# Kernel tuning notes

Hardware: AMD Instinct MI355X
Metric: run time of the kernel (lower is better)

Reference implementation:

```python
import jax, jax.numpy as jnp
import numpy as np

B, S, D, H, HD = 2, 2048, 1024, 16, 64
LN_EPS = 1e-6


def setup_inputs() -> dict:
    key = jax.random.key(0)
    ks = jax.random.split(key, 4)
    x = jax.random.normal(ks[0], (B, S, D), dtype=jnp.float32)
    ln_scale = jnp.ones((D,), jnp.float32)
    ln_bias = jnp.zeros((D,), jnp.float32)
    w_qkv = jax.random.normal(ks[1], (D, H, 3 * HD), jnp.float32) * (D ** -0.5)
    b_qkv = jnp.zeros((H, 3 * HD), jnp.float32)
    w_out = jax.random.normal(ks[2], (H, HD, D), jnp.float32) * ((H * HD) ** -0.5)
    b_out = jnp.zeros((D,), jnp.float32)
    # causal mask, broadcastable to weights shape [B, H, q, k]
    mask = jnp.tril(jnp.ones((S, S), dtype=bool))[None, None, :, :]
    return {"x": x, "ln_scale": ln_scale, "ln_bias": ln_bias,
            "w_qkv": w_qkv, "b_qkv": b_qkv, "w_out": w_out, "b_out": b_out,
            "mask": mask}


def _attention_block(x, ln_scale, ln_bias, w_qkv, b_qkv, w_out, b_out, mask):
    # Pre-LayerNorm
    mu = jnp.mean(x, axis=-1, keepdims=True)
    var = jnp.mean(jnp.square(x - mu), axis=-1, keepdims=True)
    xn = (x - mu) * jax.lax.rsqrt(var + LN_EPS) * ln_scale + ln_bias
    # QKV projection: [B,S,D] x [D,H,3*hd] -> [B,S,H,3*hd]
    qkv = jnp.einsum('bsd,dhf->bshf', xn, w_qkv) + b_qkv
    q, k, v = jnp.split(qkv, 3, axis=-1)  # each [B,S,H,hd]
    # scaled dot-product attention in float32 (softmax_dtype)
    scale = HD ** -0.5
    qf = (q * scale).astype(jnp.float32)
    kf = k.astype(jnp.float32)
    weights = jnp.einsum('bqhd,bkhd->bhqk', qf, kf)  # [B,H,S,S]
    weights = jnp.where(mask, weights, jnp.finfo(jnp.float32).min)
    weights = jax.nn.softmax(weights, axis=-1).astype(x.dtype)
    attn = jnp.einsum('bhqk,bkhd->bqhd', weights, v)  # [B,S,H,hd]
    # output projection, contracting (H, hd)
    out = jnp.einsum('bqhd,hdf->bqf', attn, w_out) + b_out  # [B,S,D]
    return out


def reference(x, ln_scale, ln_bias, w_qkv, b_qkv, w_out, b_out, mask):
    return _attention_block(x, ln_scale, ln_bias, w_qkv, b_qkv, w_out, b_out, mask)
```

## Files before the change

### kernel.cpp

```cpp
#include <hip/hip_runtime.h>
#include <hip/hip_bf16.h>
#include <stdint.h>

#define B_ 2
#define S_ 2048
#define D_ 1024
#define H_ 16
#define HD_ 64
#define M_ (B_*S_)
#define NQKV_ (H_*3*HD_)

typedef __attribute__((ext_vector_type(8))) short short8;
typedef __attribute__((ext_vector_type(4))) float f32x4;
typedef unsigned short u16;
typedef unsigned int u32;

__device__ __forceinline__ u16 f2b(float f){
  u32 u = __float_as_uint(f);
  u32 r = (u + 0x7FFFu + ((u >> 16) & 1u)) >> 16;
  return (u16)r;
}

__device__ __forceinline__ float exp2v(float x){
  float r; asm("v_exp_f32 %0, %1" : "=v"(r) : "v"(x)); return r;
}

__device__ __forceinline__ void gl_lds16(const void* g, void* l){
  __builtin_amdgcn_global_load_lds(
      (const __attribute__((address_space(1))) void*)g,
      (__attribute__((address_space(3))) void*)l, 16, 0, 0);
}

__global__ __launch_bounds__(256) void ln_kernel(const float* __restrict__ x,
    const float* __restrict__ gam, const float* __restrict__ bet, u16* __restrict__ xn){
  int row = blockIdx.x;
  const float4* xr = (const float4*)(x + (size_t)row * D_);
  float4 v = xr[threadIdx.x];
  float s = v.x + v.y + v.z + v.w;
  float q = v.x*v.x + v.y*v.y + v.z*v.z + v.w*v.w;
  #pragma unroll
  for(int o = 32; o > 0; o >>= 1){ s += __shfl_down(s, o); q += __shfl_down(q, o); }
  __shared__ float red[8];
  int w = threadIdx.x >> 6, lane = threadIdx.x & 63;
  if(lane == 0){ red[w] = s; red[4+w] = q; }
  __syncthreads();
  float st = red[0]+red[1]+red[2]+red[3];
  float qt = red[4]+red[5]+red[6]+red[7];
  float mu = st * (1.0f / D_);
  float inv = rsqrtf(qt * (1.0f / D_) - mu*mu + 1e-6f);
  float4 g = ((const float4*)gam)[threadIdx.x];
  float4 b = ((const float4*)bet)[threadIdx.x];
  ushort4 o4;
  o4.x = f2b((v.x-mu)*inv*g.x + b.x);
  o4.y = f2b((v.y-mu)*inv*g.y + b.y);
  o4.z = f2b((v.z-mu)*inv*g.z + b.z);
  o4.w = f2b((v.w-mu)*inv*g.w + b.w);
  ((ushort4*)(xn + (size_t)row * D_))[threadIdx.x] = o4;
}

__global__ __launch_bounds__(256) void tconv_kernel(const float* __restrict__ src,
    u16* __restrict__ dst, int R, int C){
  __shared__ float tile[64][65];
  int tx = threadIdx.x & 63, ty = threadIdx.x >> 6;
  int r0 = blockIdx.y * 64, c0 = blockIdx.x * 64;
  #pragma unroll
  for(int i = 0; i < 16; i++){
    int r = ty*16 + i;
    tile[r][tx] = src[(size_t)(r0+r)*C + c0 + tx];
  }
  __syncthreads();
  #pragma unroll
  for(int i = 0; i < 16; i++){
    int r = ty*16 + i;
    dst[(size_t)(c0+r)*R + r0 + tx] = f2b(tile[tx][r]);
  }
}

__global__ __launch_bounds__(256) void vtrans_kernel(const u16* __restrict__ V, u16* __restrict__ Vt){
  __shared__ u16 t2[64][66];
  int tx = threadIdx.x & 63, ty = threadIdx.x >> 6;
  int bh = blockIdx.y, s0 = blockIdx.x * 64;
  const u16* src = V + (size_t)bh * S_ * HD_;
  u16* dst = Vt + (size_t)bh * HD_ * S_;
  #pragma unroll
  for(int i = 0; i < 16; i++){
    int r = ty*16 + i;
    t2[r][tx] = src[(size_t)(s0+r)*HD_ + tx];
  }
  __syncthreads();
  #pragma unroll
  for(int i = 0; i < 16; i++){
    int hd = ty*16 + i;
    dst[(size_t)hd*S_ + s0 + tx] = t2[tx][hd];
  }
}

__global__ __launch_bounds__(512, 2) void gemm256_kernel(const u16* __restrict__ A,
    const u16* __restrict__ Bt, const float* __restrict__ bias,
    u16* __restrict__ o0, u16* __restrict__ o1, u16* __restrict__ o2){
  constexpr int K_ = 1024;
  __shared__ __align__(16) char smem[131072];
  int tid = threadIdx.x, w = tid >> 6, lane = tid & 63;
  int wm = w >> 2, wn = w & 3;
  int bid = blockIdx.y * gridDim.x + blockIdx.x;
  int nwg = gridDim.x * gridDim.y;
  int cpx = nwg >> 3;
  int swz = (bid & 7) * cpx + (bid >> 3);
  int m0 = (swz / gridDim.x) * 256, n0 = (swz % gridDim.x) * 256;

  f32x4 z = {0.f, 0.f, 0.f, 0.f};
  f32x4 acc[8][4];
  #pragma unroll
  for(int r = 0; r < 8; r++)
    #pragma unroll
    for(int c = 0; c < 4; c++) acc[r][c] = z;

  int srow_lo = w*8 + (lane >> 3);
  int sch = (lane & 7) ^ (srow_lo & 7);
  auto STAGE_A = [&](int buf, int half, int kt){
    #pragma unroll
    for(int l = 0; l < 2; l++){
      int row = l*64 + srow_lo;
      gl_lds16(A + (size_t)(m0 + half*128 + row)*K_ + kt*64 + sch*8,
               smem + (buf*2 + half)*16384 + l*8192 + w*1024);
    }
  };
  auto STAGE_B = [&](int buf, int half, int kt){
    #pragma unroll
    for(int l = 0; l < 2; l++){
      int row = l*64 + srow_lo;
      gl_lds16(Bt + (size_t)(n0 + half*128 + row)*K_ + kt*64 + sch*8,
               smem + 65536 + (buf*2 + half)*16384 + l*8192 + w*1024);
    }
  };

  int ln15 = lane & 15, g = lane >> 4;
  int co0 = ((g    ) ^ (ln15 & 7)) * 16;
  int co1 = ((4 + g) ^ (ln15 & 7)) * 16;
  auto LDA = [&](int buf, int r, int k)->short8{
    int byt = buf*32768 + wm*16384 + (r*16 + ln15)*128 + (k ? co1 : co0);
    return *(const short8*)(smem + byt);
  };
  auto LDB = [&](int buf, int c, int k)->short8{
    int byt = 65536 + buf*32768 + (wn >> 1)*16384
            + ((wn & 1)*64 + c*16 + ln15)*128 + (k ? co1 : co0);
    return *(const short8*)(smem + byt);
  };
  #define BAR()   __builtin_amdgcn_s_barrier()
  #define LGKM0() do{ asm volatile("s_waitcnt lgkmcnt(0)" ::: "memory"); \
                      __builtin_amdgcn_sched_barrier(0); }while(0)

  constexpr int nk = K_ / 64;
  STAGE_A(0, 0, 0); STAGE_A(0, 1, 0);
  STAGE_B(0, 0, 0); STAGE_B(0, 1, 0);
  STAGE_B(1, 0, 1); STAGE_B(1, 1, 1);
  asm volatile("s_waitcnt vmcnt(4)" ::: "memory");
  __builtin_amdgcn_sched_barrier(0);
  BAR();

  #pragma unroll 2
  for(int t = 0; t < nk; t++){
    int buf = t & 1;
    int kA = (t + 1 < nk) ? t + 1 : nk - 1;
    int kB = (t + 2 < nk) ? t + 2 : nk - 1;
    short8 a0[4][2], a1[4][2], b0[2][2], b1[2][2];
    #pragma unroll
    for(int r = 0; r < 4; r++){ a0[r][0] = LDA(buf, r, 0); a0[r][1] = LDA(buf, r, 1); }
    #pragma unroll
    for(int c = 0; c < 2; c++){ b0[c][0] = LDB(buf, c, 0); b0[c][1] = LDB(buf, c, 1); }
    STAGE_A(buf ^ 1, 0, kA);
    BAR(); LGKM0();
    __builtin_amdgcn_s_setprio(1);
    #pragma unroll
    for(int r = 0; r < 4; r++)
      #pragma unroll
      for(int c = 0; c < 2; c++){
        acc[r][c] = __builtin_amdgcn_mfma_f32_16x16x32_bf16(a0[r][0], b0[c][0], acc[r][c], 0, 0, 0);
        acc[r][c] = __builtin_amdgcn_mfma_f32_16x16x32_bf16(a0[r][1], b0[c][1], acc[r][c], 0, 0, 0);
      }
    __builtin_amdgcn_s_setprio(0);
    BAR();
    #pragma unroll
    for(int c = 0; c < 2; c++){ b1[c][0] = LDB(buf, c + 2, 0); b1[c][1] = LDB(buf, c + 2, 1); }
    STAGE_A(buf ^ 1, 1, kA);
    BAR(); LGKM0();
    __builtin_amdgcn_s_setprio(1);
    #pragma unroll
    for(int r = 0; r < 4; r++)
      #pragma unroll
      for(int c = 0; c < 2; c++){
        acc[r][c+2] = __builtin_amdgcn_mfma_f32_16x16x32_bf16(a0[r][0], b1[c][0], acc[r][c+2], 0, 0, 0);
        acc[r][c+2] = __builtin_amdgcn_mfma_f32_16x16x32_bf16(a0[r][1], b1[c][1], acc[r][c+2], 0, 0, 0);
      }
    __builtin_amdgcn_s_setprio(0);
    BAR();
    #pragma unroll
    for(int r = 0; r < 4; r++){ a1[r][0] = LDA(buf, r + 4, 0); a1[r][1] = LDA(buf, r + 4, 1); }
    STAGE_B(buf, 0, kB);
    BAR(); LGKM0();
    __builtin_amdgcn_s_setprio(1);
    #pragma unroll
    for(int r = 0; r < 4; r++)
      #pragma unroll
      for(int c = 0; c < 2; c++){
        acc[r+4][c+2] = __builtin_amdgcn_mfma_f32_16x16x32_bf16(a1[r][0], b1[c][0], acc[r+4][c+2], 0, 0, 0);
        acc[r+4][c+2] = __builtin_amdgcn_mfma_f32_16x16x32_bf16(a1[r][1], b1[c][1], acc[r+4][c+2], 0, 0, 0);
      }
    __builtin_amdgcn_s_setprio(0);
    BAR();
    STAGE_B(buf, 1, kB);
    BAR();
    __builtin_amdgcn_s_setprio(1);
    #pragma unroll
    for(int r = 0; r < 4; r++)
      #pragma unroll
      for(int c = 0; c < 2; c++){
        acc[r+4][c] = __builtin_amdgcn_mfma_f32_16x16x32_bf16(a1[r][0], b0[c][0], acc[r+4][c], 0, 0, 0);
        acc[r+4][c] = __builtin_amdgcn_mfma_f32_16x16x32_bf16(a1[r][1], b0[c][1], acc[r+4][c], 0, 0, 0);
      }
    __builtin_amdgcn_s_setprio(0);
    asm volatile("s_waitcnt vmcnt(4)" ::: "memory");
    __builtin_amdgcn_sched_barrier(0);
    BAR();
  }
  #undef BAR
  #undef LGKM0

  #pragma unroll
  for(int r = 0; r < 8; r++){
    #pragma unroll
    for(int c = 0; c < 4; c++){
      #pragma unroll
      for(int q = 0; q < 4; q++){
        int row = m0 + wm*128 + r*16 + g*4 + q;
        int col = n0 + wn*64 + c*16 + ln15;
        float v = acc[r][c][q] + bias[col];
        int h = col / 192, rr = col - h*192;
        int b = row >> 11, s = row & (S_ - 1);
        size_t base = ((size_t)(b*H_ + h)*S_ + s) * HD_;
        if(rr < 64)        o0[base + rr]       = f2b(v * 0.180336884f);
        else if(rr < 128)  o1[base + rr - 64]  = f2b(v);
        else               o2[base + rr - 128] = f2b(v);
      }
    }
  }
}

__global__ __launch_bounds__(256) void gemm_kernel(const u16* __restrict__ A,
    const u16* __restrict__ Bt, const float* __restrict__ bias,
    float* __restrict__ out, int K, int N){
  __shared__ u16 As[2][128*32];
  __shared__ u16 Bs[2][128*32];
  int tid = threadIdx.x, w = tid >> 6, lane = tid & 63;
  int bid = blockIdx.y * gridDim.x + blockIdx.x;
  int nwg = gridDim.x * gridDim.y;
  int cpx = nwg >> 3;
  int swz = (bid & 7) * cpx + (bid >> 3);
  int m0 = (swz / gridDim.x) * 128, n0 = (swz % gridDim.x) * 128;
  int wm = w >> 1, wn = w & 1;
  f32x4 z = {0.f, 0.f, 0.f, 0.f};
  f32x4 acc[4][4];
  #pragma unroll
  for(int r = 0; r < 4; r++)
    #pragma unroll
    for(int c = 0; c < 4; c++) acc[r][c] = z;
  int srow = lane >> 2, sch = (lane & 3) * 8;
  const u16* Ag = A + (size_t)m0 * K + (size_t)srow * K + sch;
  const u16* Bg = Bt + (size_t)n0 * K + (size_t)srow * K + sch;

  auto STAGE = [&](int buf, int kt){
    #pragma unroll
    for(int i = 0; i < 2; i++){
      int rb = w*32 + i*16;
      gl_lds16(Ag + (size_t)rb*K + kt, &As[buf][rb*32]);
      gl_lds16(Bg + (size_t)rb*K + kt, &Bs[buf][rb*32]);
    }
  };

  int nk = K >> 5;
  STAGE(0, 0);
  asm volatile("s_waitcnt vmcnt(0)" ::: "memory");
  __builtin_amdgcn_sched_barrier(0);
  __builtin_amdgcn_s_barrier();
  for(int t = 0; t < nk; t++){
    int cur = t & 1;
    if(t + 1 < nk){
      STAGE(cur ^ 1, (t + 1) * 32);
      asm volatile("s_waitcnt vmcnt(4)" ::: "memory");
    } else {
      asm volatile("s_waitcnt vmcnt(0)" ::: "memory");
    }
    __builtin_amdgcn_sched_barrier(0);
    __builtin_amdgcn_s_barrier();
    int kc = (lane >> 4) * 8;
    int ar = wm*64 + (lane & 15);
    int bc = wn*64 + (lane & 15);
    short8 af[4], bfr[4];
    #pragma unroll
    for(int r = 0; r < 4; r++) af[r] = *(const short8*)&As[cur][(ar + r*16)*32 + kc];
    #pragma unroll
    for(int c = 0; c < 4; c++) bfr[c] = *(const short8*)&Bs[cur][(bc + c*16)*32 + kc];
    __builtin_amdgcn_s_setprio(1);
    #pragma unroll
    for(int r = 0; r < 4; r++)
      #pragma unroll
      for(int c = 0; c < 4; c++)
        acc[r][c] = __builtin_amdgcn_mfma_f32_16x16x32_bf16(af[r], bfr[c], acc[r][c], 0, 0, 0);
    __builtin_amdgcn_s_setprio(0);
    asm volatile("" ::: "memory");
    __builtin_amdgcn_s_barrier();
  }

  #pragma unroll
  for(int r = 0; r < 4; r++){
    #pragma unroll
    for(int c = 0; c < 4; c++){
      #pragma unroll
      for(int q = 0; q < 4; q++){
        int row = m0 + wm*64 + r*16 + (lane >> 4)*4 + q;
        int col = n0 + wn*64 + c*16 + (lane & 15);
        out[(size_t)row * N + col] = acc[r][c][q] + bias[col];
      }
    }
  }
}


template<int HALF>
__device__ __forceinline__ void compute_tile(
    const char* KsB, const char* VsB, char* Pw, const short8* qf,
    f32x4* o, float& m_run, float& l_run, bool diag, int lane, int wr){
  constexpr int KB0 = (HALF == 1) ? 2 : 0;
  constexpr int KBN = (HALF == -1) ? 4 : 2;
  f32x4 z = {0.f, 0.f, 0.f, 0.f};
  f32x4 sf[4];
  __builtin_amdgcn_s_setprio(1);
  #pragma unroll
  for(int kb = KB0; kb < KB0 + KBN; kb++){
    f32x4 acc = z;
    #pragma unroll
    for(int c = 0; c < 2; c++){
      int row = kb*16 + (lane & 15);
      int kc16 = (lane >> 4) + c*4;
      short8 kf = *(const short8*)(KsB + row*128 + ((kc16 ^ (row & 7)) * 16));
      acc = __builtin_amdgcn_mfma_f32_16x16x32_bf16(kf, qf[c], acc, 0, 0, 0);
    }
    sf[kb] = acc;
  }
  __builtin_amdgcn_s_setprio(0);
  if(diag){
    int qo = wr*16 + (lane & 15);
    #pragma unroll
    for(int kb = KB0; kb < KB0 + KBN; kb++)
      #pragma unroll
      for(int r = 0; r < 4; r++){
        int kvo = kb*16 + (lane >> 4)*4 + r;
        if(kvo > qo) sf[kb][r] = -1e30f;
      }
  }
  int g = lane >> 4;
  float pmax = -1e28f;
  #pragma unroll
  for(int kb = KB0; kb < KB0 + KBN; kb++)
    pmax = fmaxf(pmax, fmaxf(fmaxf(sf[kb][0], sf[kb][1]), fmaxf(sf[kb][2], sf[kb][3])));
  pmax = fmaxf(pmax, __shfl_xor(pmax, 16));
  pmax = fmaxf(pmax, __shfl_xor(pmax, 32));
  if(!__all(pmax <= m_run + 8.f)){
    float mn = fmaxf(m_run, pmax);
    float al = exp2v(m_run - mn);
    m_run = mn;
    l_run *= al;
    float alr[4];
    #pragma unroll
    for(int r = 0; r < 4; r++) alr[r] = __shfl(al, g*4 + r);
    #pragma unroll
    for(int n = 0; n < 4; n++)
      #pragma unroll
      for(int r = 0; r < 4; r++) o[n][r] *= alr[r];
  }
  float p[4][4];
  float sum = 0.f;
  #pragma unroll
  for(int kb = KB0; kb < KB0 + KBN; kb++){
    #pragma unroll
    for(int r = 0; r < 4; r++) p[kb][r] = exp2v(sf[kb][r] - m_run);
    sum += (p[kb][0]+p[kb][1]) + (p[kb][2]+p[kb][3]);
  }
  sum += __shfl_xor(sum, 16);
  sum += __shfl_xor(sum, 32);
  l_run += sum;
  int qrow = lane & 15;
  #pragma unroll
  for(int kb = KB0; kb < KB0 + KBN; kb++){
    u32 lo, hi;
    asm("v_cvt_pk_bf16_f32 %0, %1, %2" : "=v"(lo) : "v"(p[kb][0]), "v"(p[kb][1]));
    asm("v_cvt_pk_bf16_f32 %0, %1, %2" : "=v"(hi) : "v"(p[kb][2]), "v"(p[kb][3]));
    uint2 pk; pk.x = lo; pk.y = hi;
    int byt = (qrow*128 + kb*32 + g*8) ^ ((qrow & 7) << 4);
    *(uint2*)(Pw + byt) = pk;
  }
  constexpr int C0 = (HALF == 1) ? 1 : 0;
  constexpr int C1 = (HALF == 0) ? 0 : 1;
  __builtin_amdgcn_s_setprio(1);
  #pragma unroll
  for(int c = C0; c <= C1; c++){
    int prow = lane & 15;
    int kb16 = ((lane >> 4) + c*4) * 16;
    short8 pa = *(const short8*)(Pw + ((prow*128 + kb16) ^ ((prow & 7) << 4)));
    #pragma unroll
    for(int n = 0; n < 4; n++){
      int vrow = n*16 + (lane & 15);
      int kc16 = (lane >> 4) + c*4;
      short8 vf = *(const short8*)(VsB + vrow*128 + ((kc16 ^ (vrow & 7)) * 16));
      o[n] = __builtin_amdgcn_mfma_f32_16x16x32_bf16(pa, vf, o[n], 0, 0, 0);
    }
  }
  __builtin_amdgcn_s_setprio(0);
}

__global__ __launch_bounds__(512) void attn_kernel(const u16* __restrict__ Q,
    const u16* __restrict__ Kb, const u16* __restrict__ Vt, u16* __restrict__ O){
  __shared__ __align__(16) char smem[49152];
  char* PsBase = smem + 32768;
  int tid = threadIdx.x, w = tid >> 6, lane = tid & 63;
  int wr = w & 3, role = w >> 2;
  int L = blockIdx.x;
  int pi = (L >> 3) & 15;
  int bh = (L & 7) + 8 * (L >> 7);
  const int NT = S_ / 64;
  int ta = pi, tb = NT - 1 - pi;
  const u16* Qg = Q + (size_t)bh * S_ * HD_;
  const u16* Kg = Kb + (size_t)bh * S_ * HD_;
  const u16* Vg = Vt + (size_t)bh * HD_ * S_;
  int b = bh >> 4, h = bh & 15;

  short8 qb[2], qa[2];
  {
    int rb_ = tb*64 + wr*16 + (lane & 15);
    #pragma unroll
    for(int c = 0; c < 2; c++)
      qb[c] = *(const short8*)(Qg + (size_t)rb_*HD_ + (lane >> 4)*8 + c*32);
    if(role == 1){
      int ra_ = ta*64 + wr*16 + (lane & 15);
      #pragma unroll
      for(int c = 0; c < 2; c++)
        qa[c] = *(const short8*)(Qg + (size_t)ra_*HD_ + (lane >> 4)*8 + c*32);
    }
  }
  f32x4 z = {0.f, 0.f, 0.f, 0.f};
  f32x4 o[4];
  float m_run = -1e30f, l_run = 0.f;
  #pragma unroll
  for(int i = 0; i < 4; i++) o[i] = z;
  int svrow = lane >> 3, scb = lane & 7;

  auto STAGE = [&](int buf, int kt){
    int kv0 = kt * 64;
    int rowblk = w * 8;
    int row = rowblk + svrow;
    int cbs = scb ^ (row & 7);
    gl_lds16(Kg + (size_t)(kv0 + row)*HD_ + cbs*8, smem + buf*8192 + rowblk*128);
    gl_lds16(Vg + (size_t)row*S_ + kv0 + cbs*8, smem + 16384 + buf*8192 + rowblk*128);
  };

  STAGE(0, 0);
  asm volatile("s_waitcnt vmcnt(0)" ::: "memory");
  __builtin_amdgcn_sched_barrier(0);
  __builtin_amdgcn_s_barrier();
  int cur = 0;
  char* Pw = PsBase + w*2048;
  for(int kt = 0; kt <= tb; kt++){
    if(kt < tb){
      STAGE(cur ^ 1, kt + 1);
      asm volatile("s_waitcnt vmcnt(2)" ::: "memory");
    } else {
      asm volatile("s_waitcnt vmcnt(0)" ::: "memory");
    }
    __builtin_amdgcn_sched_barrier(0);
    __builtin_amdgcn_s_barrier();
    const char* KsB = (const char*)(smem + cur*8192);
    const char* VsB = (const char*)(smem + 16384 + cur*8192);
    if(role == 0){
      if(kt <= ta) compute_tile<-1>(KsB, VsB, Pw, qb, o, m_run, l_run, false, lane, wr);
      else         compute_tile<0>(KsB, VsB, Pw, qb, o, m_run, l_run, kt == tb, lane, wr);
    } else {
      if(kt <= ta){
        compute_tile<-1>(KsB, VsB, Pw, qa, o, m_run, l_run, kt == ta, lane, wr);
        if(kt == ta){
          float linv = 1.f / l_run;
          float invr[4];
          #pragma unroll
          for(int r = 0; r < 4; r++) invr[r] = __shfl(linv, (lane >> 4)*4 + r);
          #pragma unroll
          for(int n = 0; n < 4; n++)
            #pragma unroll
            for(int r = 0; r < 4; r++){
              int s = ta*64 + wr*16 + (lane >> 4)*4 + r;
              int hd = n*16 + (lane & 15);
              O[(((size_t)(b*S_ + s))*H_ + h)*HD_ + hd] = f2b(o[n][r] * invr[r]);
            }
          m_run = -1e30f; l_run = 0.f;
          #pragma unroll
          for(int i = 0; i < 4; i++) o[i] = z;
        }
      } else {
        compute_tile<1>(KsB, VsB, Pw, qb, o, m_run, l_run, kt == tb, lane, wr);
      }
    }
    asm volatile("" ::: "memory");
    __builtin_amdgcn_s_barrier();
    cur ^= 1;
  }

  float* Mg = (float*)smem + wr*1072;
  if(role == 1){
    #pragma unroll
    for(int n = 0; n < 4; n++)
      #pragma unroll
      for(int r = 0; r < 4; r++)
        Mg[((lane >> 4)*4 + r)*65 + n*16 + (lane & 15)] = o[n][r];
    if(lane < 16){ Mg[1040 + lane] = m_run; Mg[1056 + lane] = l_run; }
  }
  __syncthreads();
  if(role == 0){
    float F1[4], F2[4], den[4];
    #pragma unroll
    for(int r = 0; r < 4; r++){
      int row = (lane >> 4)*4 + r;
      float m1r = __shfl(m_run, row);
      float l1r = __shfl(l_run, row);
      float m2r = Mg[1040 + row];
      float l2r = Mg[1056 + row];
      float mm = fmaxf(m1r, m2r);
      F1[r] = exp2v(m1r - mm);
      F2[r] = exp2v(m2r - mm);
      den[r] = 1.f / (l1r*F1[r] + l2r*F2[r]);
    }
    #pragma unroll
    for(int n = 0; n < 4; n++)
      #pragma unroll
      for(int r = 0; r < 4; r++){
        int row = (lane >> 4)*4 + r;
        float o2 = Mg[row*65 + n*16 + (lane & 15)];
        float val = (o[n][r]*F1[r] + o2*F2[r]) * den[r];
        int s = tb*64 + wr*16 + row;
        int hd = n*16 + (lane & 15);
        O[(((size_t)(b*S_ + s))*H_ + h)*HD_ + hd] = f2b(val);
      }
  }
}

extern "C" void kernel_launch(void* const* d_in, const int* in_sizes, int n_in,
                              void* d_out, int out_size, void* d_ws, size_t ws_size,
                              hipStream_t stream){
  (void)in_sizes; (void)n_in; (void)out_size; (void)ws_size;
  const float* x    = (const float*)d_in[0];
  const float* gam  = (const float*)d_in[1];
  const float* bet  = (const float*)d_in[2];
  const float* wqkv = (const float*)d_in[3];
  const float* bqkv = (const float*)d_in[4];
  const float* wout = (const float*)d_in[5];
  const float* bout = (const float*)d_in[6];
  char* ws = (char*)d_ws;
  u16* xn    = (u16*)(ws);
  u16* wqkvT = (u16*)(ws + 8388608);
  u16* woutT = (u16*)(ws + 8388608 + 6291456);
  u16* Qb    = (u16*)(ws + 16777216);
  u16* Kb    = (u16*)(ws + 16777216 + 8388608);
  u16* Vb    = (u16*)(ws + 16777216 + 2*8388608);
  u16* Vt    = (u16*)(ws + 16777216 + 3*8388608);
  u16* attnb = xn;
  float* out = (float*)d_out;

  ln_kernel<<<dim3(M_), dim3(256), 0, stream>>>(x, gam, bet, xn);
  tconv_kernel<<<dim3(NQKV_/64, D_/64), dim3(256), 0, stream>>>(wqkv, wqkvT, D_, NQKV_);
  tconv_kernel<<<dim3(D_/64, D_/64), dim3(256), 0, stream>>>(wout, woutT, D_, D_);
  gemm256_kernel<<<dim3(NQKV_/256, M_/256), dim3(512), 0, stream>>>(xn, wqkvT, bqkv, Qb, Kb, Vb);
  vtrans_kernel<<<dim3(S_/64, B_*H_), dim3(256), 0, stream>>>(Vb, Vt);
  attn_kernel<<<dim3(512), dim3(512), 0, stream>>>(Qb, Kb, Vt, attnb);
  gemm_kernel<<<dim3(D_/128, M_/128), dim3(256), 0, stream>>>(attnb, woutT, bout, out, D_, D_);
}
```

Before: 128.4 us.

## Stage two KV tiles per barrier and defer softmax row-sum reduction

The attention loop now stages 128 KV rows (two 64-row sub-tiles) per iteration into larger double-buffered LDS, with a 16-way swizzle for V, and processes both sub-tiles between one pair of barriers. This halves the number of barriers and waitcnt stalls per row of work. The cross-lane shuffle reduction of the softmax sum now runs only at finalisation instead of every tile, since the per-lane partial sums are all rescaled by the same factor. LDS use grows from 48KB to 80KB per block, which may reduce occupancy, and an odd tile count leaves half of the last staged buffer unused.

Result: slower. 137.1 us (+6.8%).

```diff
diff --git a/kernel.cpp b/kernel.cpp
--- a/kernel.cpp
+++ b/kernel.cpp
@@ -329,7 +329,7 @@
 template<int HALF>
 __device__ __forceinline__ void compute_tile(
     const char* KsB, const char* VsB, char* Pw, const short8* qf,
-    f32x4* o, float& m_run, float& l_run, bool diag, int lane, int wr){
+    f32x4* o, float& m_run, float& l_run, bool diag, int lane, int wr, int sub){
   constexpr int KB0 = (HALF == 1) ? 2 : 0;
   constexpr int KBN = (HALF == -1) ? 4 : 2;
   f32x4 z = {0.f, 0.f, 0.f, 0.f};
@@ -342,7 +342,7 @@
     for(int c = 0; c < 2; c++){
       int row = kb*16 + (lane & 15);
       int kc16 = (lane >> 4) + c*4;
-      short8 kf = *(const short8*)(KsB + row*128 + ((kc16 ^ (row & 7)) * 16));
+      short8 kf = *(const short8*)(KsB + sub*8192 + row*128 + ((kc16 ^ (row & 7)) * 16));
       acc = __builtin_amdgcn_mfma_f32_16x16x32_bf16(kf, qf[c], acc, 0, 0, 0);
     }
     sf[kb] = acc;
@@ -386,8 +386,6 @@
     for(int r = 0; r < 4; r++) p[kb][r] = exp2v(sf[kb][r] - m_run);
     sum += (p[kb][0]+p[kb][1]) + (p[kb][2]+p[kb][3]);
   }
-  sum += __shfl_xor(sum, 16);
-  sum += __shfl_xor(sum, 32);
   l_run += sum;
   int qrow = lane & 15;
   #pragma unroll
@@ -410,8 +408,8 @@
     #pragma unroll
     for(int n = 0; n < 4; n++){
       int vrow = n*16 + (lane & 15);
-      int kc16 = (lane >> 4) + c*4;
-      short8 vf = *(const short8*)(VsB + vrow*128 + ((kc16 ^ (vrow & 7)) * 16));
+      int kc16 = sub*8 + (lane >> 4) + c*4;
+      short8 vf = *(const short8*)(VsB + vrow*256 + ((kc16 ^ (vrow & 15)) * 16));
       o[n] = __builtin_amdgcn_mfma_f32_16x16x32_bf16(pa, vf, o[n], 0, 0, 0);
     }
   }
@@ -420,8 +418,8 @@
 
 __global__ __launch_bounds__(512) void attn_kernel(const u16* __restrict__ Q,
     const u16* __restrict__ Kb, const u16* __restrict__ Vt, u16* __restrict__ O){
-  __shared__ __align__(16) char smem[49152];
-  char* PsBase = smem + 32768;
+  __shared__ __align__(16) char smem[81920];
+  char* PsBase = smem + 65536;
   int tid = threadIdx.x, w = tid >> 6, lane = tid & 63;
   int wr = w & 3, role = w >> 2;
   int L = blockIdx.x;
@@ -452,66 +450,87 @@
   float m_run = -1e30f, l_run = 0.f;
   #pragma unroll
   for(int i = 0; i < 4; i++) o[i] = z;
-  int svrow = lane >> 3, scb = lane & 7;
-
-  auto STAGE = [&](int buf, int kt){
-    int kv0 = kt * 64;
-    int rowblk = w * 8;
-    int row = rowblk + svrow;
-    int cbs = scb ^ (row & 7);
-    gl_lds16(Kg + (size_t)(kv0 + row)*HD_ + cbs*8, smem + buf*8192 + rowblk*128);
-    gl_lds16(Vg + (size_t)row*S_ + kv0 + cbs*8, smem + 16384 + buf*8192 + rowblk*128);
+
+  auto STAGE = [&](int buf, int it){
+    int kv0 = it * 128;
+    #pragma unroll
+    for(int i = 0; i < 2; i++){
+      int off = i*8192 + tid*16;
+      int krow = off >> 7;
+      int kch = ((off >> 4) & 7) ^ (krow & 7);
+      gl_lds16(Kg + (size_t)(kv0 + krow)*HD_ + kch*8, smem + buf*16384 + off);
+      int vrow = off >> 8;
+      int vch = ((off >> 4) & 15) ^ (vrow & 15);
+      gl_lds16(Vg + (size_t)vrow*S_ + kv0 + vch*8, smem + 32768 + buf*16384 + off);
+    }
   };
 
+  auto RED_L = [&](float lr)->float{
+    lr += __shfl_xor(lr, 16);
+    lr += __shfl_xor(lr, 32);
+    return lr;
+  };
+
+  int itn = (tb + 2) >> 1;
   STAGE(0, 0);
   asm volatile("s_waitcnt vmcnt(0)" ::: "memory");
   __builtin_amdgcn_sched_barrier(0);
   __builtin_amdgcn_s_barrier();
   int cur = 0;
   char* Pw = PsBase + w*2048;
-  for(int kt = 0; kt <= tb; kt++){
-    if(kt < tb){
-      STAGE(cur ^ 1, kt + 1);
-      asm volatile("s_waitcnt vmcnt(2)" ::: "memory");
+  for(int it = 0; it < itn; it++){
+    if(it + 1 < itn){
+      STAGE(cur ^ 1, it + 1);
+      asm volatile("s_waitcnt vmcnt(4)" ::: "memory");
     } else {
       asm volatile("s_waitcnt vmcnt(0)" ::: "memory");
     }
     __builtin_amdgcn_sched_barrier(0);
     __builtin_amdgcn_s_barrier();
-    const char* KsB = (const char*)(smem + cur*8192);
-    const char* VsB = (const char*)(smem + 16384 + cur*8192);
-    if(role == 0){
-      if(kt <= ta) compute_tile<-1>(KsB, VsB, Pw, qb, o, m_run, l_run, false, lane, wr);
-      else         compute_tile<0>(KsB, VsB, Pw, qb, o, m_run, l_run, kt == tb, lane, wr);
-    } else {
-      if(kt <= ta){
-        compute_tile<-1>(KsB, VsB, Pw, qa, o, m_run, l_run, kt == ta, lane, wr);
-        if(kt == ta){
-          float linv = 1.f / l_run;
-          float invr[4];
-          #pragma unroll
-          for(int r = 0; r < 4; r++) invr[r] = __shfl(linv, (lane >> 4)*4 + r);
-          #pragma unroll
-          for(int n = 0; n < 4; n++)
+    const char* KsB = (const char*)(smem + cur*16384);
+    const char* VsB = (const char*)(smem + 32768 + cur*16384);
+
+    auto PROCESS = [&](int kt, int sub){
+      if(role == 0){
+        if(kt <= ta) compute_tile<-1>(KsB, VsB, Pw, qb, o, m_run, l_run, false, lane, wr, sub);
+        else         compute_tile<0>(KsB, VsB, Pw, qb, o, m_run, l_run, kt == tb, lane, wr, sub);
+      } else {
+        if(kt <= ta){
+          compute_tile<-1>(KsB, VsB, Pw, qa, o, m_run, l_run, kt == ta, lane, wr, sub);
+          if(kt == ta){
+            float lt = RED_L(l_run);
+            float linv = 1.f / lt;
+            float invr[4];
             #pragma unroll
-            for(int r = 0; r < 4; r++){
-              int s = ta*64 + wr*16 + (lane >> 4)*4 + r;
-              int hd = n*16 + (lane & 15);
-              O[(((size_t)(b*S_ + s))*H_ + h)*HD_ + hd] = f2b(o[n][r] * invr[r]);
-            }
-          m_run = -1e30f; l_run = 0.f;
-          #pragma unroll
-          for(int i = 0; i < 4; i++) o[i] = z;
+            for(int r = 0; r < 4; r++) invr[r] = __shfl(linv, (lane >> 4)*4 + r);
+            #pragma unroll
+            for(int n = 0; n < 4; n++)
+              #pragma unroll
+              for(int r = 0; r < 4; r++){
+                int s = ta*64 + wr*16 + (lane >> 4)*4 + r;
+                int hd = n*16 + (lane & 15);
+                O[(((size_t)(b*S_ + s))*H_ + h)*HD_ + hd] = f2b(o[n][r] * invr[r]);
+              }
+            m_run = -1e30f; l_run = 0.f;
+            #pragma unroll
+            for(int i = 0; i < 4; i++) o[i] = z;
+          }
+        } else {
+          compute_tile<1>(KsB, VsB, Pw, qb, o, m_run, l_run, kt == tb, lane, wr, sub);
         }
-      } else {
-        compute_tile<1>(KsB, VsB, Pw, qb, o, m_run, l_run, kt == tb, lane, wr);
-      }
-    }
+      }
+    };
+
+    int kt0 = 2*it;
+    PROCESS(kt0, 0);
+    if(kt0 + 1 <= tb) PROCESS(kt0 + 1, 1);
+
     asm volatile("" ::: "memory");
     __builtin_amdgcn_s_barrier();
     cur ^= 1;
   }
 
+  float lt = RED_L(l_run);
   float* Mg = (float*)smem + wr*1072;
   if(role == 1){
     #pragma unroll
@@ -519,7 +538,7 @@
       #pragma unroll
       for(int r = 0; r < 4; r++)
         Mg[((lane >> 4)*4 + r)*65 + n*16 + (lane & 15)] = o[n][r];
-    if(lane < 16){ Mg[1040 + lane] = m_run; Mg[1056 + lane] = l_run; }
+    if(lane < 16){ Mg[1040 + lane] = m_run; Mg[1056 + lane] = lt; }
   }
   __syncthreads();
   if(role == 0){
@@ -528,7 +547,7 @@
     for(int r = 0; r < 4; r++){
       int row = (lane >> 4)*4 + r;
       float m1r = __shfl(m_run, row);
-      float l1r = __shfl(l_run, row);
+      float l1r = __shfl(lt, row);
       float m2r = Mg[1040 + row];
       float l2r = Mg[1056 + row];
       float mm = fmaxf(m1r, m2r);
```

## Retile QKV GEMM to 256x192 blocks so the grid matches CU count

Applied to the files above, without the earlier changes.

Changes the QKV projection GEMM tile from 256x256 to 256x192, giving 256 workgroups instead of 192 so every CU gets one tile. The warp layout becomes 4x2 with 64x96 per warp, B staging is split into thirds, and the MFMA/load schedule is reorganized accordingly. This targets poor CU utilization from a partial wave, at the cost of a smaller tile with lower arithmetic intensity per block and a reworked pipeline.

After: 123.0 us. 4.2% less time.

```diff
diff --git a/kernel.cpp b/kernel.cpp
--- a/kernel.cpp
+++ b/kernel.cpp
@@ -95,66 +95,63 @@
   }
 }
 
-__global__ __launch_bounds__(512, 2) void gemm256_kernel(const u16* __restrict__ A,
+__global__ __launch_bounds__(512, 1) void gemm256_kernel(const u16* __restrict__ A,
     const u16* __restrict__ Bt, const float* __restrict__ bias,
     u16* __restrict__ o0, u16* __restrict__ o1, u16* __restrict__ o2){
   constexpr int K_ = 1024;
-  __shared__ __align__(16) char smem[131072];
+  __shared__ __align__(16) char smem[114688];
   int tid = threadIdx.x, w = tid >> 6, lane = tid & 63;
-  int wm = w >> 2, wn = w & 3;
+  int wm = w >> 1, wn = w & 1;
   int bid = blockIdx.y * gridDim.x + blockIdx.x;
   int nwg = gridDim.x * gridDim.y;
   int cpx = nwg >> 3;
   int swz = (bid & 7) * cpx + (bid >> 3);
-  int m0 = (swz / gridDim.x) * 256, n0 = (swz % gridDim.x) * 256;
+  int m0 = (swz / gridDim.x) * 256, n0 = (swz % gridDim.x) * 192;
 
   f32x4 z = {0.f, 0.f, 0.f, 0.f};
-  f32x4 acc[8][4];
-  #pragma unroll
-  for(int r = 0; r < 8; r++)
-    #pragma unroll
-    for(int c = 0; c < 4; c++) acc[r][c] = z;
-
-  int srow_lo = w*8 + (lane >> 3);
-  int sch = (lane & 7) ^ (srow_lo & 7);
+  f32x4 acc[4][6];
+  #pragma unroll
+  for(int r = 0; r < 4; r++)
+    #pragma unroll
+    for(int c = 0; c < 6; c++) acc[r][c] = z;
+
+  int srow8 = tid >> 3;
+  int sch = (tid & 7) ^ (srow8 & 7);
   auto STAGE_A = [&](int buf, int half, int kt){
     #pragma unroll
     for(int l = 0; l < 2; l++){
-      int row = l*64 + srow_lo;
-      gl_lds16(A + (size_t)(m0 + half*128 + row)*K_ + kt*64 + sch*8,
-               smem + (buf*2 + half)*16384 + l*8192 + w*1024);
+      int row = half*128 + l*64 + srow8;
+      gl_lds16(A + (size_t)(m0 + row)*K_ + kt*64 + sch*8,
+               smem + buf*32768 + half*16384 + l*8192 + tid*16);
     }
   };
-  auto STAGE_B = [&](int buf, int half, int kt){
-    #pragma unroll
-    for(int l = 0; l < 2; l++){
-      int row = l*64 + srow_lo;
-      gl_lds16(Bt + (size_t)(n0 + half*128 + row)*K_ + kt*64 + sch*8,
-               smem + 65536 + (buf*2 + half)*16384 + l*8192 + w*1024);
-    }
+  auto STAGE_B3 = [&](int slot, int third, int kt){
+    int row = third*64 + srow8;
+    gl_lds16(Bt + (size_t)(n0 + row)*K_ + kt*64 + sch*8,
+             smem + 65536 + slot*24576 + third*8192 + tid*16);
   };
 
   int ln15 = lane & 15, g = lane >> 4;
   int co0 = ((g    ) ^ (ln15 & 7)) * 16;
   int co1 = ((4 + g) ^ (ln15 & 7)) * 16;
   auto LDA = [&](int buf, int r, int k)->short8{
-    int byt = buf*32768 + wm*16384 + (r*16 + ln15)*128 + (k ? co1 : co0);
-    return *(const short8*)(smem + byt);
+    int row = wm*64 + r*16 + ln15;
+    return *(const short8*)(smem + buf*32768 + row*128 + (k ? co1 : co0));
   };
-  auto LDB = [&](int buf, int c, int k)->short8{
-    int byt = 65536 + buf*32768 + (wn >> 1)*16384
-            + ((wn & 1)*64 + c*16 + ln15)*128 + (k ? co1 : co0);
-    return *(const short8*)(smem + byt);
+  auto LDB = [&](int slot, int c, int k)->short8{
+    int row = wn*96 + c*16 + ln15;
+    return *(const short8*)(smem + 65536 + slot*24576 + row*128 + (k ? co1 : co0));
   };
   #define BAR()   __builtin_amdgcn_s_barrier()
   #define LGKM0() do{ asm volatile("s_waitcnt lgkmcnt(0)" ::: "memory"); \
                       __builtin_amdgcn_sched_barrier(0); }while(0)
+  #define MF(r_, c_, a_, b_) acc[r_][c_] = __builtin_amdgcn_mfma_f32_16x16x32_bf16(a_, b_, acc[r_][c_], 0, 0, 0)
 
   constexpr int nk = K_ / 64;
   STAGE_A(0, 0, 0); STAGE_A(0, 1, 0);
-  STAGE_B(0, 0, 0); STAGE_B(0, 1, 0);
-  STAGE_B(1, 0, 1); STAGE_B(1, 1, 1);
-  asm volatile("s_waitcnt vmcnt(4)" ::: "memory");
+  STAGE_B3(0, 0, 0); STAGE_B3(0, 1, 0); STAGE_B3(0, 2, 0);
+  STAGE_B3(1, 0, 1); STAGE_B3(1, 1, 1); STAGE_B3(1, 2, 1);
+  asm volatile("s_waitcnt vmcnt(3)" ::: "memory");
   __builtin_amdgcn_sched_barrier(0);
   BAR();
 
@@ -163,77 +160,61 @@
     int buf = t & 1;
     int kA = (t + 1 < nk) ? t + 1 : nk - 1;
     int kB = (t + 2 < nk) ? t + 2 : nk - 1;
-    short8 a0[4][2], a1[4][2], b0[2][2], b1[2][2];
-    #pragma unroll
-    for(int r = 0; r < 4; r++){ a0[r][0] = LDA(buf, r, 0); a0[r][1] = LDA(buf, r, 1); }
-    #pragma unroll
-    for(int c = 0; c < 2; c++){ b0[c][0] = LDB(buf, c, 0); b0[c][1] = LDB(buf, c, 1); }
+    short8 a[4][2], b01[2][2], b23[2][2], b45[2][2];
+    #pragma unroll
+    for(int r = 0; r < 4; r++){ a[r][0] = LDA(buf, r, 0); a[r][1] = LDA(buf, r, 1); }
+    #pragma unroll
+    for(int c = 0; c < 2; c++){ b01[c][0] = LDB(buf, c, 0); b01[c][1] = LDB(buf, c, 1); }
     STAGE_A(buf ^ 1, 0, kA);
     BAR(); LGKM0();
     __builtin_amdgcn_s_setprio(1);
     #pragma unroll
     for(int r = 0; r < 4; r++)
       #pragma unroll
-      for(int c = 0; c < 2; c++){
-        acc[r][c] = __builtin_amdgcn_mfma_f32_16x16x32_bf16(a0[r][0], b0[c][0], acc[r][c], 0, 0, 0);
-        acc[r][c] = __builtin_amdgcn_mfma_f32_16x16x32_bf16(a0[r][1], b0[c][1], acc[r][c], 0, 0, 0);
-      }
+      for(int c = 0; c < 2; c++){ MF(r, c, a[r][0], b01[c][0]); MF(r, c, a[r][1], b01[c][1]); }
     __builtin_amdgcn_s_setprio(0);
     BAR();
     #pragma unroll
-    for(int c = 0; c < 2; c++){ b1[c][0] = LDB(buf, c + 2, 0); b1[c][1] = LDB(buf, c + 2, 1); }
+    for(int c = 0; c < 2; c++){ b23[c][0] = LDB(buf, c + 2, 0); b23[c][1] = LDB(buf, c + 2, 1); }
     STAGE_A(buf ^ 1, 1, kA);
     BAR(); LGKM0();
     __builtin_amdgcn_s_setprio(1);
     #pragma unroll
     for(int r = 0; r < 4; r++)
       #pragma unroll
-      for(int c = 0; c < 2; c++){
-        acc[r][c+2] = __builtin_amdgcn_mfma_f32_16x16x32_bf16(a0[r][0], b1[c][0], acc[r][c+2], 0, 0, 0);
-        acc[r][c+2] = __builtin_amdgcn_mfma_f32_16x16x32_bf16(a0[r][1], b1[c][1], acc[r][c+2], 0, 0, 0);
-      }
+      for(int c = 0; c < 2; c++){ MF(r, c+2, a[r][0], b23[c][0]); MF(r, c+2, a[r][1], b23[c][1]); }
     __builtin_amdgcn_s_setprio(0);
     BAR();
     #pragma unroll
-    for(int r = 0; r < 4; r++){ a1[r][0] = LDA(buf, r + 4, 0); a1[r][1] = LDA(buf, r + 4, 1); }
-    STAGE_B(buf, 0, kB);
+    for(int c = 0; c < 2; c++){ b45[c][0] = LDB(buf, c + 4, 0); b45[c][1] = LDB(buf, c + 4, 1); }
     BAR(); LGKM0();
     __builtin_amdgcn_s_setprio(1);
     #pragma unroll
-    for(int r = 0; r < 4; r++)
-      #pragma unroll
-      for(int c = 0; c < 2; c++){
-        acc[r+4][c+2] = __builtin_amdgcn_mfma_f32_16x16x32_bf16(a1[r][0], b1[c][0], acc[r+4][c+2], 0, 0, 0);
-        acc[r+4][c+2] = __builtin_amdgcn_mfma_f32_16x16x32_bf16(a1[r][1], b1[c][1], acc[r+4][c+2], 0, 0, 0);
-      }
+    for(int r = 0; r < 4; r++){ MF(r, 4, a[r][0], b45[0][0]); MF(r, 4, a[r][1], b45[0][1]); }
     __builtin_amdgcn_s_setprio(0);
     BAR();
-    STAGE_B(buf, 1, kB);
+    STAGE_B3(buf, 0, kB); STAGE_B3(buf, 1, kB); STAGE_B3(buf, 2, kB);
     BAR();
     __builtin_amdgcn_s_setprio(1);
     #pragma unroll
-    for(int r = 0; r < 4; r++)
-      #pragma unroll
-      for(int c = 0; c < 2; c++){
-        acc[r+4][c] = __builtin_amdgcn_mfma_f32_16x16x32_bf16(a1[r][0], b0[c][0], acc[r+4][c], 0, 0, 0);
-        acc[r+4][c] = __builtin_amdgcn_mfma_f32_16x16x32_bf16(a1[r][1], b0[c][1], acc[r+4][c], 0, 0, 0);
-      }
+    for(int r = 0; r < 4; r++){ MF(r, 5, a[r][0], b45[1][0]); MF(r, 5, a[r][1], b45[1][1]); }
     __builtin_amdgcn_s_setprio(0);
-    asm volatile("s_waitcnt vmcnt(4)" ::: "memory");
+    asm volatile("s_waitcnt vmcnt(3)" ::: "memory");
     __builtin_amdgcn_sched_barrier(0);
     BAR();
   }
   #undef BAR
   #undef LGKM0
-
-  #pragma unroll
-  for(int r = 0; r < 8; r++){
-    #pragma unroll
-    for(int c = 0; c < 4; c++){
+  #undef MF
+
+  #pragma unroll
+  for(int r = 0; r < 4; r++){
+    #pragma unroll
+    for(int c = 0; c < 6; c++){
       #pragma unroll
       for(int q = 0; q < 4; q++){
-        int row = m0 + wm*128 + r*16 + g*4 + q;
-        int col = n0 + wn*64 + c*16 + ln15;
+        int row = m0 + wm*64 + r*16 + g*4 + q;
+        int col = n0 + wn*96 + c*16 + ln15;
         float v = acc[r][c][q] + bias[col];
         int h = col / 192, rr = col - h*192;
         int b = row >> 11, s = row & (S_ - 1);
@@ -575,7 +556,7 @@
   ln_kernel<<<dim3(M_), dim3(256), 0, stream>>>(x, gam, bet, xn);
   tconv_kernel<<<dim3(NQKV_/64, D_/64), dim3(256), 0, stream>>>(wqkv, wqkvT, D_, NQKV_);
   tconv_kernel<<<dim3(D_/64, D_/64), dim3(256), 0, stream>>>(wout, woutT, D_, D_);
-  gemm256_kernel<<<dim3(NQKV_/256, M_/256), dim3(512), 0, stream>>>(xn, wqkvT, bqkv, Qb, Kb, Vb);
+  gemm256_kernel<<<dim3(NQKV_/192, M_/256), dim3(512), 0, stream>>>(xn, wqkvT, bqkv, Qb, Kb, Vb);
   vtrans_kernel<<<dim3(S_/64, B_*H_), dim3(256), 0, stream>>>(Vb, Vt);
   attn_kernel<<<dim3(512), dim3(512), 0, stream>>>(Qb, Kb, Vt, attnb);
   gemm_kernel<<<dim3(D_/128, M_/128), dim3(256), 0, stream>>>(attnb, woutT, bout, out, D_, D_);
```
